# Performance work log

Measured on AMD Instinct MI355X. Metric: run time of the kernel, lower is better.

Reference implementation:

```python
import jax, jax.numpy as jnp
import numpy as np

MEMORY_SIZE = 262144
KEY_DIM = 256
TOP_K = 256
BATCH = 256
TEMP = max(1.0, float(np.log(0.2 * TOP_K)) / 40.0)  # = 1.0
MARGIN = 0.1
AGE_NOISE = 8.0


def _normalize(v, axis=-1, eps=1e-12):
    return v / jnp.maximum(jnp.linalg.norm(v, axis=axis, keepdims=True), eps)


def setup_inputs() -> dict:
    key = jax.random.key(0)
    ks = jax.random.split(key, 5)
    x = jax.random.normal(ks[0], (BATCH, KEY_DIM), jnp.float32)
    y = jax.random.randint(ks[1], (BATCH,), 0, 1000, dtype=jnp.int32)
    W = jax.random.normal(ks[2], (KEY_DIM, KEY_DIM), jnp.float32) / np.sqrt(KEY_DIM)
    b = jnp.zeros((KEY_DIM,), jnp.float32)
    keys = _normalize(jax.random.normal(ks[3], (MEMORY_SIZE, KEY_DIM), jnp.float32), axis=1)
    values = jnp.zeros((MEMORY_SIZE, 1), jnp.int32)
    age = jnp.zeros((MEMORY_SIZE, 1), jnp.float32)
    u_noise = jax.random.uniform(ks[4], (MEMORY_SIZE, 1), jnp.float32)
    return dict(x=x, y=y, W=W, b=b, keys=keys, values=values, age=age, u_noise=u_noise)


def reference(x, y, W, b, keys, values, age, u_noise):
    # query projection + L2 normalize
    query = _normalize(x @ W.T + b, axis=1)                  # [B, D]
    scores = query @ keys.T                                  # [B, M] cosine sims
    cos_sim, topk_idx = jax.lax.top_k(scores, TOP_K)         # [B, K]
    softmax_score = jax.nn.softmax(TEMP * cos_sim, axis=-1)  # [B, K]
    y_hat_indices = topk_idx[:, 0]                           # [B]
    y_hat = values[y_hat_indices]                            # [B, 1]

    # memory loss (margin between best correct and best incorrect neighbor)
    topk_values = values[topk_idx, 0]                        # [B, K]
    correct_mask = (topk_values == y[:, None]).astype(jnp.float32)
    pos_score = jnp.max(cos_sim * correct_mask, axis=1, keepdims=True)
    neg_score = jnp.max(cos_sim * (1.0 - correct_mask), axis=1, keepdims=True)
    has_pos = (jnp.sum(correct_mask, axis=1) > 0.0).astype(jnp.float32)
    pos_score = pos_score * has_pos[:, None]
    loss = jnp.mean(jnp.maximum(neg_score - pos_score + MARGIN, 0.0))

    # ---- memory update (state buffers, no gradient) ----
    q = jax.lax.stop_gradient(query)
    correct = (y_hat[:, 0] == y)                             # [B] bool
    age = age + 1.0

    # correct examples: keys[idx] = normalize(keys[idx] + q); age[idx] = 0
    correct_dest = jnp.where(correct, y_hat_indices, MEMORY_SIZE)  # out-of-range -> dropped
    new_correct_keys = _normalize(keys[y_hat_indices] + q, axis=1)
    keys = keys.at[correct_dest].set(new_correct_keys, mode='drop')
    age = age.at[correct_dest].set(0.0, mode='drop')

    # incorrect examples: overwrite the oldest (noisy-age) memory slots
    incorrect = ~correct
    age_noisy = age[:, 0] + (2.0 * u_noise[:, 0] - 1.0) * AGE_NOISE
    _, oldest = jax.lax.top_k(age_noisy, BATCH)              # enough slots for all incorrect
    rank = jnp.cumsum(incorrect.astype(jnp.int32)) - 1       # position among incorrect
    dest = jnp.where(incorrect, oldest[jnp.maximum(rank, 0)], MEMORY_SIZE)
    keys = keys.at[dest].set(q, mode='drop')
    values = values.at[dest, 0].set(y, mode='drop')
    age = age.at[dest, 0].set(0.0, mode='drop')

    return y_hat, softmax_score, loss, keys, values, age
```

## Files before the change

kernel.cpp:

```cpp
#include <hip/hip_runtime.h>

#define MEM_N 262144
#define DIM 256
#define NBATCH 256
#define OCAP 4096
#define NSEG 8
#define SEG_SZ 32768
#define ROWCAP 2048
#define KSEL_SCORES 320
#define BPAGE 528

typedef __attribute__((ext_vector_type(8))) short short8;
typedef __attribute__((ext_vector_type(4))) float f32x4;
typedef unsigned long long u64;
typedef unsigned short u16;

__device__ __forceinline__ u16 bf16_rne(float f) {
  unsigned u = __builtin_bit_cast(unsigned, f);
  u += 0x7FFFu + ((u >> 16) & 1u);
  return (u16)(u >> 16);
}
__device__ __forceinline__ float bf16_f32(u16 h) {
  unsigned u = ((unsigned)h) << 16;
  return __builtin_bit_cast(float, u);
}
__device__ __forceinline__ u16 bf16_floor(float f) {
  unsigned u = __builtin_bit_cast(unsigned, f);
  u16 h = (u16)(u >> 16);
  if ((u & 0x80000000u) && (u & 0xFFFFu)) h++;
  return h;
}
__device__ __forceinline__ unsigned flip32(float f) {
  unsigned u = __builtin_bit_cast(unsigned, f);
  return u ^ ((unsigned)((int)u >> 31) | 0x80000000u);
}
__device__ __forceinline__ float unflip32(unsigned k) {
  unsigned u = (k & 0x80000000u) ? (k ^ 0x80000000u) : ~k;
  return __builtin_bit_cast(float, u);
}
__device__ __forceinline__ u16 flip16(u16 b) {
  return (b & 0x8000u) ? (u16)~b : (u16)(b | 0x8000u);
}
__device__ __forceinline__ u16 unflip16(u16 f) {
  return (f & 0x8000u) ? (u16)(f ^ 0x8000u) : (u16)~f;
}

__global__ __launch_bounds__(256) void k_query(
    const float* __restrict__ x, const float* __restrict__ W,
    const float* __restrict__ b, float* __restrict__ q,
    u16* __restrict__ ap_hi, u16* __restrict__ ap_lo, int* __restrict__ row_cnt,
    int* __restrict__ ocnt) {
  __shared__ float Wt[256][36];
  __shared__ float xs[256];
  __shared__ float red[256];
  const int r = blockIdx.x, t = threadIdx.x;
  if (t == 0) row_cnt[r] = 0;
  if (r == 0 && t == 0) *ocnt = 0;
  xs[t] = x[r * DIM + t];
  float acc = b[t];
  for (int k0 = 0; k0 < DIM; k0 += 32) {
    __syncthreads();
#pragma unroll
    for (int i = 0; i < 8; i++) {
      int f = i * 256 + t;
      int j = f >> 3, c = (f & 7) * 4;
      *(float4*)&Wt[j][c] = *(const float4*)&W[j * DIM + k0 + c];
    }
    __syncthreads();
#pragma unroll
    for (int c = 0; c < 32; c++) acc = fmaf(xs[k0 + c], Wt[t][c], acc);
  }
  red[t] = acc * acc;
  __syncthreads();
  for (int s = 128; s > 0; s >>= 1) {
    if (t < s) red[t] += red[t + s];
    __syncthreads();
  }
  float nrm = fmaxf(sqrtf(red[0]), 1e-12f);
  float qv = acc / nrm;
  q[r * DIM + t] = qv;
  u16 h = bf16_rne(qv);
  u16 lo = bf16_rne(qv - bf16_f32(h));
  int r16 = r >> 4, s = t >> 5, hi = (t >> 3) & 3, j = t & 7;
  int l = hi * 16 + (r & 15);
  size_t off = ((size_t)(r16 * 8 + s) * 64 + l) * 8 + j;
  ap_hi[off] = h;
  ap_lo[off] = lo;
}

__global__ __launch_bounds__(512, 4) void k_gemm(
    const u16* __restrict__ ap_hi, const u16* __restrict__ ap_lo,
    const float* __restrict__ keys, float* __restrict__ scores,
    u16* __restrict__ rowmax) {
  __shared__ __align__(16) unsigned char smem[67584];
  u16* Bf = (u16*)smem;
  const int t = threadIdx.x;
  const int cb = blockIdx.x;
  const int slot0 = cb * 128;
  const int w = t >> 6, l = t & 63;
  const int wm = w & 3, wn = w >> 2;
  const int lrow = l & 15, lq = l >> 4;
  const int srow = t >> 2, sk = t & 3;
  const float* kp = keys + (size_t)(slot0 + srow) * DIM + sk * 8;
  const int sbase = (srow >> 6) * (16 * BPAGE);
  const int scol = srow & 63;

  f32x4 acc[4][4];
#pragma unroll
  for (int i = 0; i < 4; ++i)
#pragma unroll
    for (int j = 0; j < 4; ++j) acc[i][j] = f32x4{0.f, 0.f, 0.f, 0.f};

  {
    float4 va[4][2];
#pragma unroll
    for (int j = 0; j < 4; j++) {
      va[j][0] = *(const float4*)(kp + j * 32);
      va[j][1] = *(const float4*)(kp + j * 32 + 4);
    }
#pragma unroll
    for (int j = 0; j < 4; j++) {
      float f0[8] = {va[j][0].x, va[j][0].y, va[j][0].z, va[j][0].w,
                     va[j][1].x, va[j][1].y, va[j][1].z, va[j][1].w};
      uint4 pk;
      unsigned* pw = (unsigned*)&pk;
#pragma unroll
      for (int i = 0; i < 4; i++)
        pw[i] = (unsigned)bf16_rne(f0[2 * i]) | ((unsigned)bf16_rne(f0[2 * i + 1]) << 16);
      *(uint4*)&Bf[sbase + (j * 4 + sk) * BPAGE + scol * 8] = pk;
    }
  }
  __syncthreads();
#pragma unroll
  for (int ksl = 0; ksl < 4; ksl++) {
    short8 bh[4], ah[4], al[4];
#pragma unroll
    for (int nf = 0; nf < 4; nf++)
      bh[nf] = *(const short8*)(&Bf[wn * (16 * BPAGE) + (ksl * 4 + lq) * BPAGE + (nf * 16 + lrow) * 8]);
#pragma unroll
    for (int mf = 0; mf < 4; mf++) {
      size_t ab = ((size_t)((wm * 4 + mf) * 8 + ksl) * 64 + l) * 8;
      ah[mf] = *(const short8*)(ap_hi + ab);
      al[mf] = *(const short8*)(ap_lo + ab);
    }
#pragma unroll
    for (int mf = 0; mf < 4; mf++)
#pragma unroll
      for (int nf = 0; nf < 4; nf++) {
        acc[mf][nf] = __builtin_amdgcn_mfma_f32_16x16x32_bf16(al[mf], bh[nf], acc[mf][nf], 0, 0, 0);
        acc[mf][nf] = __builtin_amdgcn_mfma_f32_16x16x32_bf16(ah[mf], bh[nf], acc[mf][nf], 0, 0, 0);
      }
  }
  float4 vb[4][2];
#pragma unroll
  for (int j = 0; j < 4; j++) {
    vb[j][0] = *(const float4*)(kp + 128 + j * 32);
    vb[j][1] = *(const float4*)(kp + 128 + j * 32 + 4);
  }
  __syncthreads();
#pragma unroll
  for (int j = 0; j < 4; j++) {
    float f0[8] = {vb[j][0].x, vb[j][0].y, vb[j][0].z, vb[j][0].w,
                   vb[j][1].x, vb[j][1].y, vb[j][1].z, vb[j][1].w};
    uint4 pk;
    unsigned* pw = (unsigned*)&pk;
#pragma unroll
    for (int i = 0; i < 4; i++)
      pw[i] = (unsigned)bf16_rne(f0[2 * i]) | ((unsigned)bf16_rne(f0[2 * i + 1]) << 16);
    *(uint4*)&Bf[sbase + (j * 4 + sk) * BPAGE + scol * 8] = pk;
  }
  __syncthreads();
#pragma unroll
  for (int ksl = 0; ksl < 4; ksl++) {
    short8 bh[4], ah[4], al[4];
#pragma unroll
    for (int nf = 0; nf < 4; nf++)
      bh[nf] = *(const short8*)(&Bf[wn * (16 * BPAGE) + (ksl * 4 + lq) * BPAGE + (nf * 16 + lrow) * 8]);
#pragma unroll
    for (int mf = 0; mf < 4; mf++) {
      size_t ab = ((size_t)((wm * 4 + mf) * 8 + 4 + ksl) * 64 + l) * 8;
      ah[mf] = *(const short8*)(ap_hi + ab);
      al[mf] = *(const short8*)(ap_lo + ab);
    }
#pragma unroll
    for (int mf = 0; mf < 4; mf++)
#pragma unroll
      for (int nf = 0; nf < 4; nf++) {
        acc[mf][nf] = __builtin_amdgcn_mfma_f32_16x16x32_bf16(al[mf], bh[nf], acc[mf][nf], 0, 0, 0);
        acc[mf][nf] = __builtin_amdgcn_mfma_f32_16x16x32_bf16(ah[mf], bh[nf], acc[mf][nf], 0, 0, 0);
      }
  }

#pragma unroll
  for (int mf = 0; mf < 4; mf++)
#pragma unroll
    for (int j = 0; j < 4; j++) {
      float m = fmaxf(fmaxf(acc[mf][0][j], acc[mf][1][j]),
                      fmaxf(acc[mf][2][j], acc[mf][3][j]));
#pragma unroll
      for (int mk = 1; mk <= 8; mk <<= 1) m = fmaxf(m, __shfl_xor(m, mk));
      if ((l & 15) == 0) {
        int row = wm * 64 + mf * 16 + lq * 4 + j;
        rowmax[(size_t)row * 4096 + cb * 2 + wn] = bf16_floor(m);
      }
    }

  float* trb = (float*)smem;
#pragma unroll
  for (int rd = 0; rd < 2; rd++) {
    __syncthreads();
#pragma unroll
    for (int hh = 0; hh < 2; hh++) {
      int mf = rd * 2 + hh;
      float* tr2 = trb + (hh * 8 + w) * 1056;
#pragma unroll
      for (int nf = 0; nf < 4; nf++)
#pragma unroll
        for (int j = 0; j < 4; j++)
          tr2[(lq * 4 + j) * 66 + nf * 16 + lrow] = acc[mf][nf][j];
    }
    __syncthreads();
#pragma unroll
    for (int hh = 0; hh < 2; hh++) {
      int mf = rd * 2 + hh;
      float* tr2 = trb + (hh * 8 + w) * 1056;
#pragma unroll
      for (int it = 0; it < 4; it++) {
        float4 vv = *(float4*)&tr2[(it * 4 + lq) * 66 + 4 * lrow];
        size_t row = (size_t)(wm * 64 + mf * 16 + it * 4 + lq);
        *(float4*)&scores[row * MEM_N + slot0 + wn * 64 + 4 * lrow] = vv;
      }
    }
  }
}

__global__ __launch_bounds__(256) void k_cut(
    const u16* __restrict__ rowmax, float* __restrict__ cut_row, int ksel) {
  __shared__ int h[256];
  __shared__ int Bsh, Lsh;
  const int r = blockIdx.x, t = threadIdx.x;
  const u16* rm = rowmax + (size_t)r * 4096;
  uint4 a0 = *(const uint4*)(rm + t * 16);
  uint4 a1 = *(const uint4*)(rm + t * 16 + 8);
  u16 f[16];
  unsigned aw[8] = {a0.x, a0.y, a0.z, a0.w, a1.x, a1.y, a1.z, a1.w};
#pragma unroll
  for (int i = 0; i < 8; i++) {
    f[2 * i] = flip16((u16)(aw[i] & 0xFFFFu));
    f[2 * i + 1] = flip16((u16)(aw[i] >> 16));
  }
  h[t] = 0;
  __syncthreads();
#pragma unroll
  for (int i = 0; i < 16; i++) atomicAdd(&h[f[i] >> 8], 1);
  __syncthreads();
  for (int off = 1; off < 256; off <<= 1) {
    int v = (t + off < 256) ? h[t + off] : 0;
    __syncthreads();
    h[t] += v;
    __syncthreads();
  }
  if (h[t] >= ksel && (t == 255 || h[t + 1] < ksel)) Bsh = t;
  __syncthreads();
  const int B = Bsh;
  const int above = (B == 255) ? 0 : h[B + 1];
  __syncthreads();
  h[t] = 0;
  __syncthreads();
#pragma unroll
  for (int i = 0; i < 16; i++)
    if ((f[i] >> 8) == B) atomicAdd(&h[f[i] & 255], 1);
  __syncthreads();
  for (int off = 1; off < 256; off <<= 1) {
    int v = (t + off < 256) ? h[t + off] : 0;
    __syncthreads();
    h[t] += v;
    __syncthreads();
  }
  if (above + h[t] >= ksel && (t == 255 || above + h[t + 1] < ksel)) Lsh = t;
  __syncthreads();
  if (t == 0) {
    u16 fs = (u16)((B << 8) | Lsh);
    cut_row[r] = bf16_f32(unflip16(fs));
  }
}

__device__ void bitonic_desc(u64* a, int N, int t) {
  for (int k = 2; k <= N; k <<= 1) {
    for (int j = k >> 1; j > 0; j >>= 1) {
      for (int i = t; i < N; i += 256) {
        int p = i ^ j;
        if (p > i) {
          u64 xv = a[i], yv = a[p];
          bool up = ((i & k) == 0);
          if (up ? (xv < yv) : (xv > yv)) { a[i] = yv; a[p] = xv; }
        }
      }
      __syncthreads();
    }
  }
}

__global__ __launch_bounds__(256) void k_sweep(
    const float* __restrict__ scores, const float* __restrict__ cut_row,
    const u16* __restrict__ rowmax, const float* __restrict__ keys,
    u64* __restrict__ cand_row, int* __restrict__ row_cnt,
    float* __restrict__ keys_out) {
  __shared__ u64 lbuf[2048];
  __shared__ u16 sblk[512];
  __shared__ int lcnt, nsb, gbase;
  const int seg = blockIdx.x, r = blockIdx.y, t = threadIdx.x;
  if (t == 0) { lcnt = 0; nsb = 0; }
  __syncthreads();
  const float cutval = cut_row[r];
  const float* p = scores + (size_t)r * MEM_N + (size_t)seg * SEG_SZ;

  const u16* rm = rowmax + (size_t)r * 4096 + seg * 512;
#pragma unroll
  for (int i2 = 0; i2 < 2; i2++) {
    int i = t * 2 + i2;
    if (bf16_f32(rm[i]) >= cutval) {
      int pz = atomicAdd(&nsb, 1);
      sblk[pz] = (u16)i;
    }
  }
  __syncthreads();
  const int ns = nsb;
  for (int i0 = 0; i0 < ns; i0 += 16) {
    int ib = i0 + (t >> 4);
    if (ib < ns) {
      int b = sblk[ib];
      int off = b * 64 + (t & 15) * 4;
      float4 v = *(const float4*)(p + off);
      float vv[4] = {v.x, v.y, v.z, v.w};
      int c0 = seg * SEG_SZ + off;
#pragma unroll
      for (int e = 0; e < 4; e++) {
        if (vv[e] >= cutval) {
          u64 key = (((u64)flip32(vv[e])) << 32) | (unsigned)(~(unsigned)(c0 + e));
          int pz = atomicAdd(&lcnt, 1);
          if (pz < 2048) lbuf[pz] = key;
        }
      }
    }
  }
  __syncthreads();
  int n = lcnt < 2048 ? lcnt : 2048;
  if (t == 0) gbase = atomicAdd(&row_cnt[r], n);
  __syncthreads();
  const int gb = gbase;
  u64* crow = cand_row + (size_t)r * ROWCAP;
  for (int i = t; i < n; i += 256) {
    int gp = gb + i;
    if (gp < ROWCAP) crow[gp] = lbuf[i];
  }

  const long long b = (long long)r * MEM_N + (long long)seg * SEG_SZ - 1;
  for (int i = t; i < 8192; i += 256) {
    long long k4 = b + 4LL * i;
    if (k4 < 0) continue;
    float s = keys[k4];
    float4 v = *(const float4*)(keys + k4 + 1);
    float4 o;
    o.x = s; o.y = v.x; o.z = v.y; o.w = v.z;
    *(float4*)(keys_out + k4) = o;
  }
  if (r == 0 && seg == 0 && t == 0) {
    keys_out[0] = keys[0]; keys_out[1] = keys[1]; keys_out[2] = keys[2];
  }
}

__global__ __launch_bounds__(256) void k_topk2(
    const u64* __restrict__ cand_row, const int* __restrict__ row_cnt,
    const int* __restrict__ values, const int* __restrict__ yv,
    const float* __restrict__ keys, const float* __restrict__ q,
    float* __restrict__ out, float* __restrict__ loss_arr,
    int* __restrict__ corr, float* __restrict__ age_out,
    float* __restrict__ keys_out) {
  __shared__ u64 buf[ROWCAP];
  __shared__ float red[256];
  const int r = blockIdx.x, t = threadIdx.x;
  if (r == 255 && t == 32) {
    const long long N = (long long)MEM_N * DIM;
    keys_out[N - 1] = keys[N - 1];
  }
  int cnt = row_cnt[r];
  cnt = cnt < ROWCAP ? cnt : ROWCAP;
  int S = 256;
  while (S < cnt) S <<= 1;
  const u64* src = cand_row + (size_t)r * ROWCAP;
  for (int i = t; i < S; i += 256) buf[i] = (i < cnt) ? src[i] : 0ULL;
  __syncthreads();
  bitonic_desc(buf, S, t);

  u64 mykey = buf[t];
  int midx = (int)(~(unsigned)(mykey & 0xFFFFFFFFull));
  float msc = unflip32((unsigned)(mykey >> 32));
  int yr = yv[r];
  float mask = (values[midx] == yr) ? 1.0f : 0.0f;
  float mtop = unflip32((unsigned)(buf[0] >> 32));
  int i0 = (int)(~(unsigned)(buf[0] & 0xFFFFFFFFull));
  int vi0 = values[i0];
  bool correct = (vi0 == yr);

  float e = expf(msc - mtop);
  red[t] = e; __syncthreads();
  for (int s = 128; s > 0; s >>= 1) { if (t < s) red[t] += red[t + s]; __syncthreads(); }
  float denom = red[0]; __syncthreads();
  out[256 + r * 256 + t] = e / denom;

  red[t] = msc * mask; __syncthreads();
  for (int s = 128; s > 0; s >>= 1) { if (t < s) red[t] = fmaxf(red[t], red[t + s]); __syncthreads(); }
  float posr = red[0]; __syncthreads();

  red[t] = msc * (1.0f - mask); __syncthreads();
  for (int s = 128; s > 0; s >>= 1) { if (t < s) red[t] = fmaxf(red[t], red[t + s]); __syncthreads(); }
  float negr = red[0]; __syncthreads();

  red[t] = mask; __syncthreads();
  for (int s = 128; s > 0; s >>= 1) { if (t < s) red[t] += red[t + s]; __syncthreads(); }
  float hp = (red[0] > 0.0f) ? 1.0f : 0.0f;
  __syncthreads();

  if (t == 0) {
    float pos = posr * hp;
    loss_arr[r] = fmaxf(negr - pos + 0.1f, 0.0f);
    out[r] = (float)vi0;
    corr[r] = correct ? 1 : 0;
  }
  if (correct) {
    if (t == 0) age_out[i0] = 0.0f;
    float v = keys[(size_t)i0 * DIM + t] + q[r * DIM + t];
    red[t] = v * v; __syncthreads();
    for (int s = 128; s > 0; s >>= 1) { if (t < s) red[t] += red[t + s]; __syncthreads(); }
    float nrm = fmaxf(sqrtf(red[0]), 1e-12f);
    keys_out[(size_t)i0 * DIM + t] = v / nrm;
  }
}

__global__ __launch_bounds__(256) void k_age(
    const float* __restrict__ age, const int* __restrict__ values,
    float* __restrict__ age_out, float* __restrict__ vals_out) {
  int i = blockIdx.x * 256 + threadIdx.x;
  age_out[i] = age[i] + 1.0f;
  vals_out[i] = (float)values[i];
}

__global__ __launch_bounds__(256) void k_oldmax(
    const float* __restrict__ age_out, const float* __restrict__ un,
    u16* __restrict__ old_max) {
  const int t = threadIdx.x, bid = blockIdx.x;
  int g = bid * 1024 + t * 4;
  float4 a = *(const float4*)(age_out + g);
  float4 n4 = *(const float4*)(un + g);
  float m = a.x + (2.0f * n4.x - 1.0f) * 8.0f;
  m = fmaxf(m, a.y + (2.0f * n4.y - 1.0f) * 8.0f);
  m = fmaxf(m, a.z + (2.0f * n4.z - 1.0f) * 8.0f);
  m = fmaxf(m, a.w + (2.0f * n4.w - 1.0f) * 8.0f);
#pragma unroll
  for (int mk = 1; mk <= 8; mk <<= 1) m = fmaxf(m, __shfl_xor(m, mk));
  if ((t & 15) == 0) old_max[bid * 16 + (t >> 4)] = bf16_floor(m);
}

__global__ __launch_bounds__(256) void k_oldsweep(
    const float* __restrict__ age_out, const float* __restrict__ un,
    const float* __restrict__ old_cut, u64* __restrict__ obuf,
    int* __restrict__ ocnt) {
  const int t = threadIdx.x, bid = blockIdx.x;
  int g = bid * 1024 + t * 4;
  const float cut = *old_cut;
  float4 a = *(const float4*)(age_out + g);
  float4 n4 = *(const float4*)(un + g);
  float av[4] = {a.x, a.y, a.z, a.w};
  float nv[4] = {n4.x, n4.y, n4.z, n4.w};
#pragma unroll
  for (int e = 0; e < 4; e++) {
    float v = av[e] + (2.0f * nv[e] - 1.0f) * 8.0f;
    if (v >= cut) {
      u64 k = (((u64)flip32(v)) << 32) | (unsigned)(~(unsigned)(g + e));
      int p = atomicAdd(ocnt, 1);
      if (p < OCAP) obuf[p] = k;
    }
  }
}

__global__ __launch_bounds__(256) void k_oldB(
    const u64* __restrict__ obuf, const int* __restrict__ ocnt,
    const int* __restrict__ corr, const float* __restrict__ loss_arr,
    int* __restrict__ dest, float* __restrict__ out_loss) {
  __shared__ u64 cand[OCAP];
  __shared__ int olds[256];
  __shared__ int pre[256];
  __shared__ float red[256];
  const int t = threadIdx.x;
  int n = *ocnt;
  n = n < OCAP ? n : OCAP;
  int S = 256;
  while (S < n) S <<= 1;
  for (int i = t; i < S; i += 256) cand[i] = (i < n) ? obuf[i] : 0ULL;
  __syncthreads();
  bitonic_desc(cand, S, t);
  olds[t] = (int)(~(unsigned)(cand[t] & 0xFFFFFFFFull));
  int inc = corr[t] ? 0 : 1;
  pre[t] = inc;
  __syncthreads();
  for (int off = 1; off < 256; off <<= 1) {
    int v = (t >= off) ? pre[t - off] : 0;
    __syncthreads();
    pre[t] += v;
    __syncthreads();
  }
  int rank = pre[t] - 1;
  dest[t] = inc ? olds[rank] : -1;
  red[t] = loss_arr[t]; __syncthreads();
  for (int s = 128; s > 0; s >>= 1) { if (t < s) red[t] += red[t + s]; __syncthreads(); }
  if (t == 0) *out_loss = red[0] * (1.0f / 256.0f);
}

__global__ __launch_bounds__(256) void k_incorrect(
    const int* __restrict__ dest, const float* __restrict__ q,
    const int* __restrict__ yv, float* __restrict__ keys_out,
    float* __restrict__ vals_out, float* __restrict__ age_out) {
  const int r = blockIdx.x;
  int d = dest[r];
  if (d < 0) return;
  const int t = threadIdx.x;
  keys_out[(size_t)d * DIM + t] = q[r * DIM + t];
  if (t == 0) {
    vals_out[d] = (float)yv[r];
    age_out[d] = 0.0f;
  }
}

extern "C" void kernel_launch(void* const* d_in, const int* in_sizes, int n_in,
                              void* d_out, int out_size, void* d_ws, size_t ws_size,
                              hipStream_t stream) {
  const float* x = (const float*)d_in[0];
  const int* y = (const int*)d_in[1];
  const float* W = (const float*)d_in[2];
  const float* b = (const float*)d_in[3];
  const float* keys = (const float*)d_in[4];
  const int* values = (const int*)d_in[5];
  const float* age = (const float*)d_in[6];
  const float* un = (const float*)d_in[7];
  float* out = (float*)d_out;

  char* ws = (char*)d_ws;
  float* q = (float*)ws;
  u16* ap_hi = (u16*)(ws + 262144);
  u16* ap_lo = (u16*)(ws + 393216);
  float* loss_arr = (float*)(ws + 524288);
  int* corr = (int*)(ws + 525312);
  u64* obuf = (u64*)(ws + 527360);
  int* dest = (int*)(ws + 560128);
  int* row_cnt = (int*)(ws + 561152);
  float* cut_row = (float*)(ws + 562176);
  u16* old_max = (u16*)(ws + 563200);
  float* old_cut = (float*)(ws + 571392);
  int* ocnt = (int*)(ws + 571648);
  u64* cand_row = (u64*)(ws + 1048576);

  const size_t LOSS_OFF = 65792, KEYS_OFF = 65793, VALS_OFF = 67174657,
               AGE_OFF = 67436801;
  float* scores = out + 65792;
  u16* rowmax = (u16*)(out + 67174656);
  float* keys_out = out + KEYS_OFF;
  float* vals_out = out + VALS_OFF;
  float* age_out = out + AGE_OFF;

  k_query<<<dim3(256), dim3(256), 0, stream>>>(x, W, b, q, ap_hi, ap_lo, row_cnt, ocnt);
  k_gemm<<<dim3(2048), dim3(512), 0, stream>>>(ap_hi, ap_lo, keys, scores, rowmax);
  k_cut<<<dim3(256), dim3(256), 0, stream>>>(rowmax, cut_row, KSEL_SCORES);
  k_sweep<<<dim3(NSEG, 256), dim3(256), 0, stream>>>(scores, cut_row, rowmax, keys, cand_row, row_cnt, keys_out);
  k_age<<<dim3(1024), dim3(256), 0, stream>>>(age, values, age_out, vals_out);
  k_topk2<<<dim3(256), dim3(256), 0, stream>>>(cand_row, row_cnt, values, y, keys, q,
                                               out, loss_arr, corr, age_out, keys_out);
  k_oldmax<<<dim3(256), dim3(256), 0, stream>>>(age_out, un, old_max);
  k_cut<<<dim3(1), dim3(256), 0, stream>>>(old_max, old_cut, 256);
  k_oldsweep<<<dim3(256), dim3(256), 0, stream>>>(age_out, un, old_cut, obuf, ocnt);
  k_oldB<<<dim3(1), dim3(256), 0, stream>>>(obuf, ocnt, corr, loss_arr, dest, out + LOSS_OFF);
  k_incorrect<<<dim3(256), dim3(256), 0, stream>>>(dest, q, y, keys_out, vals_out, age_out);
}
```

Measured before the change: 404.9 us.

## Fuse keys copy into GEMM and move scores scratch to workspace

Adds a GEMM variant that also writes the unaligned keys copy to the output while it stages keys for the MFMA tiles, so the sweep kernel no longer re-reads and re-writes all keys. Scores and rowmax now go to a large workspace region instead of the output buffer, and a slimmer sweep kernel only selects candidates. This path runs only when the workspace is at least about 276 MB; otherwise the old path is kept. The packed unaligned stores may be slower than the aligned float4 shifted copy, and the larger GEMM epilogue adds register pressure.

```diff
diff --git a/kernel.cpp b/kernel.cpp
--- a/kernel.cpp
+++ b/kernel.cpp
@@ -14,6 +14,8 @@
 typedef __attribute__((ext_vector_type(4))) float f32x4;
 typedef unsigned long long u64;
 typedef unsigned short u16;
+
+struct __attribute__((packed)) f4u { float x, y, z, w; };
 
 __device__ __forceinline__ u16 bf16_rne(float f) {
   unsigned u = __builtin_bit_cast(unsigned, f);
@@ -87,6 +89,7 @@
   ap_hi[off] = h;
   ap_lo[off] = lo;
 }
+
 
 __global__ __launch_bounds__(512, 4) void k_gemm(
     const u16* __restrict__ ap_hi, const u16* __restrict__ ap_lo,
@@ -234,6 +237,163 @@
   }
 }
 
+__global__ __launch_bounds__(512, 4) void k_gemm_f(
+    const u16* __restrict__ ap_hi, const u16* __restrict__ ap_lo,
+    const float* __restrict__ keys, float* __restrict__ scores,
+    u16* __restrict__ rowmax, float* __restrict__ keys_out) {
+  __shared__ __align__(16) unsigned char smem[67584];
+  u16* Bf = (u16*)smem;
+  const int t = threadIdx.x;
+  const int cb = blockIdx.x;
+  const int slot0 = cb * 128;
+  const int w = t >> 6, l = t & 63;
+  const int wm = w & 3, wn = w >> 2;
+  const int lrow = l & 15, lq = l >> 4;
+  const int srow = t >> 2, sk = t & 3;
+  const float* kp = keys + (size_t)(slot0 + srow) * DIM + sk * 8;
+  float* op = keys_out + ((size_t)(slot0 + srow) * DIM + sk * 8);
+  const int sbase = (srow >> 6) * (16 * BPAGE);
+  const int scol = srow & 63;
+
+  f32x4 acc[4][4];
+#pragma unroll
+  for (int i = 0; i < 4; ++i)
+#pragma unroll
+    for (int j = 0; j < 4; ++j) acc[i][j] = f32x4{0.f, 0.f, 0.f, 0.f};
+
+  {
+    float4 va[4][2];
+#pragma unroll
+    for (int j = 0; j < 4; j++) {
+      va[j][0] = *(const float4*)(kp + j * 32);
+      va[j][1] = *(const float4*)(kp + j * 32 + 4);
+    }
+#pragma unroll
+    for (int j = 0; j < 4; j++) {
+      float f0[8] = {va[j][0].x, va[j][0].y, va[j][0].z, va[j][0].w,
+                     va[j][1].x, va[j][1].y, va[j][1].z, va[j][1].w};
+      uint4 pk;
+      unsigned* pw = (unsigned*)&pk;
+#pragma unroll
+      for (int i = 0; i < 4; i++)
+        pw[i] = (unsigned)bf16_rne(f0[2 * i]) | ((unsigned)bf16_rne(f0[2 * i + 1]) << 16);
+      *(uint4*)&Bf[sbase + (j * 4 + sk) * BPAGE + scol * 8] = pk;
+    }
+#pragma unroll
+    for (int j = 0; j < 4; j++) {
+      *(f4u*)(op + j * 32) = f4u{va[j][0].x, va[j][0].y, va[j][0].z, va[j][0].w};
+      *(f4u*)(op + j * 32 + 4) = f4u{va[j][1].x, va[j][1].y, va[j][1].z, va[j][1].w};
+    }
+  }
+  __syncthreads();
+#pragma unroll
+  for (int ksl = 0; ksl < 4; ksl++) {
+    short8 bh[4], ah[4], al[4];
+#pragma unroll
+    for (int nf = 0; nf < 4; nf++)
+      bh[nf] = *(const short8*)(&Bf[wn * (16 * BPAGE) + (ksl * 4 + lq) * BPAGE + (nf * 16 + lrow) * 8]);
+#pragma unroll
+    for (int mf = 0; mf < 4; mf++) {
+      size_t ab = ((size_t)((wm * 4 + mf) * 8 + ksl) * 64 + l) * 8;
+      ah[mf] = *(const short8*)(ap_hi + ab);
+      al[mf] = *(const short8*)(ap_lo + ab);
+    }
+#pragma unroll
+    for (int mf = 0; mf < 4; mf++)
+#pragma unroll
+      for (int nf = 0; nf < 4; nf++) {
+        acc[mf][nf] = __builtin_amdgcn_mfma_f32_16x16x32_bf16(al[mf], bh[nf], acc[mf][nf], 0, 0, 0);
+        acc[mf][nf] = __builtin_amdgcn_mfma_f32_16x16x32_bf16(ah[mf], bh[nf], acc[mf][nf], 0, 0, 0);
+      }
+  }
+  float4 vb[4][2];
+#pragma unroll
+  for (int j = 0; j < 4; j++) {
+    vb[j][0] = *(const float4*)(kp + 128 + j * 32);
+    vb[j][1] = *(const float4*)(kp + 128 + j * 32 + 4);
+  }
+#pragma unroll
+  for (int j = 0; j < 4; j++) {
+    *(f4u*)(op + 128 + j * 32) = f4u{vb[j][0].x, vb[j][0].y, vb[j][0].z, vb[j][0].w};
+    *(f4u*)(op + 128 + j * 32 + 4) = f4u{vb[j][1].x, vb[j][1].y, vb[j][1].z, vb[j][1].w};
+  }
+  __syncthreads();
+#pragma unroll
+  for (int j = 0; j < 4; j++) {
+    float f0[8] = {vb[j][0].x, vb[j][0].y, vb[j][0].z, vb[j][0].w,
+                   vb[j][1].x, vb[j][1].y, vb[j][1].z, vb[j][1].w};
+    uint4 pk;
+    unsigned* pw = (unsigned*)&pk;
+#pragma unroll
+    for (int i = 0; i < 4; i++)
+      pw[i] = (unsigned)bf16_rne(f0[2 * i]) | ((unsigned)bf16_rne(f0[2 * i + 1]) << 16);
+    *(uint4*)&Bf[sbase + (j * 4 + sk) * BPAGE + scol * 8] = pk;
+  }
+  __syncthreads();
+#pragma unroll
+  for (int ksl = 0; ksl < 4; ksl++) {
+    short8 bh[4], ah[4], al[4];
+#pragma unroll
+    for (int nf = 0; nf < 4; nf++)
+      bh[nf] = *(const short8*)(&Bf[wn * (16 * BPAGE) + (ksl * 4 + lq) * BPAGE + (nf * 16 + lrow) * 8]);
+#pragma unroll
+    for (int mf = 0; mf < 4; mf++) {
+      size_t ab = ((size_t)((wm * 4 + mf) * 8 + 4 + ksl) * 64 + l) * 8;
+      ah[mf] = *(const short8*)(ap_hi + ab);
+      al[mf] = *(const short8*)(ap_lo + ab);
+    }
+#pragma unroll
+    for (int mf = 0; mf < 4; mf++)
+#pragma unroll
+      for (int nf = 0; nf < 4; nf++) {
+        acc[mf][nf] = __builtin_amdgcn_mfma_f32_16x16x32_bf16(al[mf], bh[nf], acc[mf][nf], 0, 0, 0);
+        acc[mf][nf] = __builtin_amdgcn_mfma_f32_16x16x32_bf16(ah[mf], bh[nf], acc[mf][nf], 0, 0, 0);
+      }
+  }
+
+#pragma unroll
+  for (int mf = 0; mf < 4; mf++)
+#pragma unroll
+    for (int j = 0; j < 4; j++) {
+      float m = fmaxf(fmaxf(acc[mf][0][j], acc[mf][1][j]),
+                      fmaxf(acc[mf][2][j], acc[mf][3][j]));
+#pragma unroll
+      for (int mk = 1; mk <= 8; mk <<= 1) m = fmaxf(m, __shfl_xor(m, mk));
+      if ((l & 15) == 0) {
+        int row = wm * 64 + mf * 16 + lq * 4 + j;
+        rowmax[(size_t)row * 4096 + cb * 2 + wn] = bf16_floor(m);
+      }
+    }
+
+  float* trb = (float*)smem;
+#pragma unroll
+  for (int rd = 0; rd < 2; rd++) {
+    __syncthreads();
+#pragma unroll
+    for (int hh = 0; hh < 2; hh++) {
+      int mf = rd * 2 + hh;
+      float* tr2 = trb + (hh * 8 + w) * 1056;
+#pragma unroll
+      for (int nf = 0; nf < 4; nf++)
+#pragma unroll
+        for (int j = 0; j < 4; j++)
+          tr2[(lq * 4 + j) * 66 + nf * 16 + lrow] = acc[mf][nf][j];
+    }
+    __syncthreads();
+#pragma unroll
+    for (int hh = 0; hh < 2; hh++) {
+      int mf = rd * 2 + hh;
+      float* tr2 = trb + (hh * 8 + w) * 1056;
+#pragma unroll
+      for (int it = 0; it < 4; it++) {
+        float4 vv = *(float4*)&tr2[(it * 4 + lq) * 66 + 4 * lrow];
+        size_t row = (size_t)(wm * 64 + mf * 16 + it * 4 + lq);
+        *(float4*)&scores[row * MEM_N + slot0 + wn * 64 + 4 * lrow] = vv;
+      }
+    }
+  }
+}
+
 __global__ __launch_bounds__(256) void k_cut(
     const u16* __restrict__ rowmax, float* __restrict__ cut_row, int ksel) {
   __shared__ int h[256];
@@ -367,6 +527,59 @@
   }
   if (r == 0 && seg == 0 && t == 0) {
     keys_out[0] = keys[0]; keys_out[1] = keys[1]; keys_out[2] = keys[2];
+  }
+}
+
+__global__ __launch_bounds__(256) void k_sweep_s(
+    const float* __restrict__ scores, const float* __restrict__ cut_row,
+    const u16* __restrict__ rowmax, u64* __restrict__ cand_row,
+    int* __restrict__ row_cnt) {
+  __shared__ u64 lbuf[2048];
+  __shared__ u16 sblk[512];
+  __shared__ int lcnt, nsb, gbase;
+  const int seg = blockIdx.x, r = blockIdx.y, t = threadIdx.x;
+  if (t == 0) { lcnt = 0; nsb = 0; }
+  __syncthreads();
+  const float cutval = cut_row[r];
+  const float* p = scores + (size_t)r * MEM_N + (size_t)seg * SEG_SZ;
+  const u16* rm = rowmax + (size_t)r * 4096 + seg * 512;
+#pragma unroll
+  for (int i2 = 0; i2 < 2; i2++) {
+    int i = t * 2 + i2;
+    if (bf16_f32(rm[i]) >= cutval) {
+      int pz = atomicAdd(&nsb, 1);
+      sblk[pz] = (u16)i;
+    }
+  }
+  __syncthreads();
+  const int ns = nsb;
+  for (int i0 = 0; i0 < ns; i0 += 16) {
+    int ib = i0 + (t >> 4);
+    if (ib < ns) {
+      int b = sblk[ib];
+      int off = b * 64 + (t & 15) * 4;
+      float4 v = *(const float4*)(p + off);
+      float vv[4] = {v.x, v.y, v.z, v.w};
+      int c0 = seg * SEG_SZ + off;
+#pragma unroll
+      for (int e = 0; e < 4; e++) {
+        if (vv[e] >= cutval) {
+          u64 key = (((u64)flip32(vv[e])) << 32) | (unsigned)(~(unsigned)(c0 + e));
+          int pz = atomicAdd(&lcnt, 1);
+          if (pz < 2048) lbuf[pz] = key;
+        }
+      }
+    }
+  }
+  __syncthreads();
+  int n = lcnt < 2048 ? lcnt : 2048;
+  if (t == 0) gbase = atomicAdd(&row_cnt[r], n);
+  __syncthreads();
+  const int gb = gbase;
+  u64* crow = cand_row + (size_t)r * ROWCAP;
+  for (int i = t; i < n; i += 256) {
+    int gp = gb + i;
+    if (gp < ROWCAP) crow[gp] = lbuf[i];
   }
 }
 
@@ -562,16 +775,27 @@
 
   const size_t LOSS_OFF = 65792, KEYS_OFF = 65793, VALS_OFF = 67174657,
                AGE_OFF = 67436801;
-  float* scores = out + 65792;
-  u16* rowmax = (u16*)(out + 67174656);
   float* keys_out = out + KEYS_OFF;
   float* vals_out = out + VALS_OFF;
   float* age_out = out + AGE_OFF;
 
+  const size_t NEED_LARGE = 8388608ull + 268435456ull;
+  const bool large = (ws_size >= NEED_LARGE);
+
   k_query<<<dim3(256), dim3(256), 0, stream>>>(x, W, b, q, ap_hi, ap_lo, row_cnt, ocnt);
-  k_gemm<<<dim3(2048), dim3(512), 0, stream>>>(ap_hi, ap_lo, keys, scores, rowmax);
-  k_cut<<<dim3(256), dim3(256), 0, stream>>>(rowmax, cut_row, KSEL_SCORES);
-  k_sweep<<<dim3(NSEG, 256), dim3(256), 0, stream>>>(scores, cut_row, rowmax, keys, cand_row, row_cnt, keys_out);
+  if (large) {
+    u16* rowmax = (u16*)(ws + 6291456);
+    float* scores = (float*)(ws + 8388608);
+    k_gemm_f<<<dim3(2048), dim3(512), 0, stream>>>(ap_hi, ap_lo, keys, scores, rowmax, keys_out);
+    k_cut<<<dim3(256), dim3(256), 0, stream>>>(rowmax, cut_row, KSEL_SCORES);
+    k_sweep_s<<<dim3(NSEG, 256), dim3(256), 0, stream>>>(scores, cut_row, rowmax, cand_row, row_cnt);
+  } else {
+    float* scores = out + 65792;
+    u16* rowmax = (u16*)(out + 67174656);
+    k_gemm<<<dim3(2048), dim3(512), 0, stream>>>(ap_hi, ap_lo, keys, scores, rowmax);
+    k_cut<<<dim3(256), dim3(256), 0, stream>>>(rowmax, cut_row, KSEL_SCORES);
+    k_sweep<<<dim3(NSEG, 256), dim3(256), 0, stream>>>(scores, cut_row, rowmax, keys, cand_row, row_cnt, keys_out);
+  }
   k_age<<<dim3(1024), dim3(256), 0, stream>>>(age, values, age_out, vals_out);
   k_topk2<<<dim3(256), dim3(256), 0, stream>>>(cand_row, row_cnt, values, y, keys, q,
                                                out, loss_arr, corr, age_out, keys_out);
```

Measured after the change: 396.0 us. 2.2% less time.
